# Kernel tuning notes

Hardware: AMD Instinct MI355X
Metric: run time of the kernel (lower is better)

## Reference

```python
import jax, jax.numpy as jnp
import numpy as np

H = 24
HEAD_DIM = 128
EPS = 1e-6
IP_SCALE = 1.0

def _rms(x, w):
    return x * jax.lax.rsqrt(jnp.mean(x * x, axis=-1, keepdims=True) + EPS) * w

def _heads(x, B):
    # (B, S, H*D) -> (B, H, S, D)
    return x.reshape(B, x.shape[1], H, HEAD_DIM).transpose(0, 2, 1, 3)

def _merge(x):
    B, h, S, d = x.shape
    return x.transpose(0, 2, 1, 3).reshape(B, S, h * d)

def _sdpa(q, k, v):
    s = jnp.einsum('bhqd,bhkd->bhqk', q, k) * (1.0 / np.sqrt(HEAD_DIM))
    return jnp.einsum('bhqk,bhkd->bhqd', jax.nn.softmax(s, axis=-1), v)

def _rope(x, cos, sin):
    # Flux-style real rotary: interleaved pairs, out = x*cos + rot(x)*sin
    xr = x.reshape(x.shape[:-1] + (-1, 2))
    x1, x2 = xr[..., 0], xr[..., 1]
    xrot = jnp.stack([-x2, x1], axis=-1).reshape(x.shape)
    return x * cos + xrot * sin

def setup_inputs():
    key = jax.random.key(0)
    ks = jax.random.split(key, 24)
    B, S_img, L_txt, D, IP_DIM, N_IP = 1, 2048, 512, 3072, 2048, 1024
    S = S_img + L_txt
    def w(k, i, o):
        return jax.random.normal(k, (i, o), jnp.float32) * 0.02
    def b(k, o):
        return jax.random.normal(k, (o,), jnp.float32) * 0.01
    pos = jnp.arange(S, dtype=jnp.float32)
    freqs = 1.0 / (10000.0 ** (jnp.arange(0, HEAD_DIM, 2, dtype=jnp.float32) / HEAD_DIM))
    ang = pos[:, None] * freqs[None, :]
    cos = jnp.repeat(jnp.cos(ang), 2, axis=-1)  # (S, HEAD_DIM)
    sin = jnp.repeat(jnp.sin(ang), 2, axis=-1)
    return {
        'hidden_states': jax.random.normal(ks[0], (B, S_img, D), jnp.float32),
        'encoder_hidden_states': jax.random.normal(ks[1], (B, L_txt, D), jnp.float32),
        'ip_hidden_states': jax.random.normal(ks[2], (B, N_IP, IP_DIM), jnp.float32),
        'rot_cos': cos, 'rot_sin': sin,
        'Wq': w(ks[3], D, D), 'bq': b(ks[4], D),
        'Wk': w(ks[5], D, D), 'bk': b(ks[6], D),
        'Wv': w(ks[7], D, D), 'bv': b(ks[8], D),
        'norm_q_w': jnp.ones((HEAD_DIM,), jnp.float32),
        'norm_k_w': jnp.ones((HEAD_DIM,), jnp.float32),
        'aWq': w(ks[9], D, D), 'abq': b(ks[10], D),
        'aWk': w(ks[11], D, D), 'abk': b(ks[12], D),
        'aWv': w(ks[13], D, D), 'abv': b(ks[14], D),
        'norm_aq_w': jnp.ones((HEAD_DIM,), jnp.float32),
        'norm_ak_w': jnp.ones((HEAD_DIM,), jnp.float32),
        'Wk_ip': w(ks[15], IP_DIM, D), 'bk_ip': b(ks[16], D),
        'Wv_ip': w(ks[17], IP_DIM, D), 'bv_ip': b(ks[18], D),
        'norm_ipq_w': jnp.ones((HEAD_DIM,), jnp.float32),
        'norm_ipk_w': jnp.ones((HEAD_DIM,), jnp.float32),
        'Wo': w(ks[19], D, D), 'bo': b(ks[20], D),
        'Wao': w(ks[21], D, D), 'bao': b(ks[22], D),
    }

def reference(hidden_states, encoder_hidden_states, ip_hidden_states, rot_cos, rot_sin,
              Wq, bq, Wk, bk, Wv, bv, norm_q_w, norm_k_w,
              aWq, abq, aWk, abk, aWv, abv, norm_aq_w, norm_ak_w,
              Wk_ip, bk_ip, Wv_ip, bv_ip, norm_ipq_w, norm_ipk_w,
              Wo, bo, Wao, bao):
    B, S_img, D = hidden_states.shape
    L = encoder_hidden_states.shape[1]
    q = _heads(hidden_states @ Wq + bq, B)   # (B,H,S_img,d)
    k = _heads(hidden_states @ Wk + bk, B)
    v = _heads(hidden_states @ Wv + bv, B)
    # IP-adapter cross-attention: RMS-normed raw image query vs projected image tokens
    ip_q = _rms(q, norm_ipq_w)
    ip_k = _rms(_heads(ip_hidden_states @ Wk_ip + bk_ip, B), norm_ipk_w)
    ip_v = _heads(ip_hidden_states @ Wv_ip + bv_ip, B)
    ip_out = _merge(_sdpa(ip_q, ip_k, ip_v))  # (B, S_img, D)
    # main joint attention with per-head QK RMSNorm
    q = _rms(q, norm_q_w)
    k = _rms(k, norm_k_w)
    eq = _rms(_heads(encoder_hidden_states @ aWq + abq, B), norm_aq_w)
    ek = _rms(_heads(encoder_hidden_states @ aWk + abk, B), norm_ak_w)
    ev = _heads(encoder_hidden_states @ aWv + abv, B)
    q = jnp.concatenate([eq, q], axis=2)
    k = jnp.concatenate([ek, k], axis=2)
    v = jnp.concatenate([ev, v], axis=2)
    q = _rope(q, rot_cos, rot_sin)
    k = _rope(k, rot_cos, rot_sin)
    hs = _merge(_sdpa(q, k, v))  # (B, L+S_img, D)
    enc = hs[:, :L]
    img = hs[:, L:] + IP_SCALE * ip_out
    img = img @ Wo + bo
    enc = enc @ Wao + bao
    return (img, enc)
```

## Files before the change

kernel.cpp:

```cpp
#include <hip/hip_runtime.h>
#include <hip/hip_bf16.h>
#include <cmath>
#include <cstdint>

#define H_    24
#define HD_   128
#define D_    3072
#define SIMG_ 2048
#define LTXT_ 512
#define SALL_ 2560
#define NIP_  1024
#define IPD_  2048

using bf16 = __hip_bfloat16;
typedef __bf16 bf16x8 __attribute__((ext_vector_type(8)));
typedef float  f32x4  __attribute__((ext_vector_type(4)));
typedef short  short8 __attribute__((ext_vector_type(8)));

#define QSCALE_ 0.12751741f

#define SWZ_BLOCK(bx, by)                                              \
  {                                                                    \
    int _gx = gridDim.x;                                               \
    int _hw = blockIdx.x + blockIdx.y * _gx;                           \
    int _n  = _gx * gridDim.y;                                         \
    int _lid = (_hw & 7) * (_n >> 3) + (_hw >> 3);                     \
    bx = _lid % _gx;                                                   \
    by = _lid / _gx;                                                   \
  }

__device__ __forceinline__ unsigned short f2bf(float f) {
  unsigned int u = __float_as_uint(f);
  unsigned int r = (u + 0x7fffu + ((u >> 16) & 1u)) >> 16;
  return (unsigned short)r;
}
__device__ __forceinline__ float bf2f(unsigned short u) {
  return __uint_as_float(((unsigned int)u) << 16);
}

__device__ __forceinline__ void gload16(const void* g, void* l) {
  __builtin_amdgcn_global_load_lds(
      (const __attribute__((address_space(1))) unsigned*)g,
      (__attribute__((address_space(3))) unsigned*)l, 16, 0, 0);
}

__global__ void cast_kernel(const float* __restrict__ x, unsigned short* __restrict__ y, int n4) {
  int i = blockIdx.x * blockDim.x + threadIdx.x;
  if (i >= n4) return;
  float4 v = reinterpret_cast<const float4*>(x)[i];
  ushort4 o = make_ushort4(f2bf(v.x), f2bf(v.y), f2bf(v.z), f2bf(v.w));
  reinterpret_cast<ushort4*>(y)[i] = o;
}

__global__ __launch_bounds__(512)
void transpose_cast3_kernel(const float* __restrict__ W0, const float* __restrict__ W1,
                            const float* __restrict__ W2, unsigned short* __restrict__ Wt,
                            int R, int C) {
  __shared__ float tile[32][69];
  const float* W = blockIdx.z == 0 ? W0 : (blockIdx.z == 1 ? W1 : W2);
  unsigned short* dst = Wt + (size_t)blockIdx.z * R * C;
  int bx = blockIdx.x * 64, by = blockIdx.y * 32;
  int tx = threadIdx.x, ty = threadIdx.y;
#pragma unroll
  for (int i = 0; i < 4; i++)
    tile[ty + 8 * i][tx] = W[(size_t)(by + ty + 8 * i) * C + bx + tx];
  __syncthreads();
  int t = ty * 64 + tx;
  int colr = t >> 3;
  int r0 = (t & 7) * 4;
  ushort4 o = make_ushort4(f2bf(tile[r0][colr]), f2bf(tile[r0 + 1][colr]),
                           f2bf(tile[r0 + 2][colr]), f2bf(tile[r0 + 3][colr]));
  *reinterpret_cast<ushort4*>(&dst[(size_t)(bx + colr) * R + by + r0]) = o;
}

__device__ __forceinline__ void gemm_core(const bf16* __restrict__ Ab, const bf16* __restrict__ Bb,
                                          int K, bf16* Alds, bf16* Blds, int t,
                                          int wid, int l16, int lg, f32x4 (&acc)[2][8]) {
  char* AldsB = (char*)Alds + t * 16;
  char* BldsB = (char*)Blds + t * 16;
  for (int kt = 0; kt < K; kt += 32) {
    __syncthreads();
    gload16(Ab + kt,                    AldsB);
    gload16(Ab + (size_t)64 * K + kt,   AldsB + 4096);
    gload16(Bb + kt,                    BldsB);
    gload16(Bb + (size_t)64 * K + kt,   BldsB + 4096);
    __syncthreads();
    bf16x8 af[2], bfr[8];
#pragma unroll
    for (int mi = 0; mi < 2; mi++)
      af[mi] = *reinterpret_cast<const bf16x8*>(&Alds[(wid * 32 + mi * 16 + l16) * 32 + lg * 8]);
#pragma unroll
    for (int ni = 0; ni < 8; ni++)
      bfr[ni] = *reinterpret_cast<const bf16x8*>(&Blds[(ni * 16 + l16) * 32 + lg * 8]);
    __builtin_amdgcn_s_setprio(1);
#pragma unroll
    for (int mi = 0; mi < 2; mi++)
#pragma unroll
      for (int ni = 0; ni < 8; ni++)
        acc[mi][ni] = __builtin_amdgcn_mfma_f32_16x16x32_bf16(af[mi], bfr[ni], acc[mi][ni], 0, 0, 0);
    __builtin_amdgcn_s_setprio(0);
  }
}

__global__ __launch_bounds__(256)
void gemm_proj_kernel(const bf16* __restrict__ A, const bf16* __restrict__ Wt,
                      int M, int K, int projmap,
                      const float* __restrict__ b0, const float* __restrict__ b1,
                      const float* __restrict__ b2,
                      const float* __restrict__ rcos, const float* __restrict__ rsin,
                      int pos_off, int tok_off, int Sout,
                      unsigned short* __restrict__ qa_p, const float* __restrict__ nq,
                      unsigned short* __restrict__ ipq_p, const float* __restrict__ nipq, int Sip,
                      unsigned short* __restrict__ ka_p, const float* __restrict__ nk,
                      unsigned short* __restrict__ va_p) {
  __shared__ __align__(16) bf16 Alds[128 * 32];
  __shared__ __align__(16) bf16 Blds[128 * 32];
  __shared__ __align__(16) bf16 VtS[64 * 128];
  int t = threadIdx.x;
  int lane = t & 63, wid = t >> 6;
  int l16 = lane & 15, lg = lane >> 4;
  int bx, by;
  SWZ_BLOCK(bx, by);
  int bm = bx * 128;
  int proj = by / 24, head = by % 24;
  int code = (projmap >> (proj * 4)) & 15;
  int arow = t >> 2, aseg = t & 3;

  f32x4 acc[2][8];
#pragma unroll
  for (int i = 0; i < 2; i++)
#pragma unroll
    for (int j = 0; j < 8; j++) { acc[i][j][0]=0.f; acc[i][j][1]=0.f; acc[i][j][2]=0.f; acc[i][j][3]=0.f; }

  const bf16* Ab = A  + (size_t)(bm + arow) * K + aseg * 8;
  const bf16* Bb = Wt + (size_t)(by * 128 + arow) * K + aseg * 8;
  gemm_core(Ab, Bb, K, Alds, Blds, t, wid, l16, lg, acc);

  const float* bias = proj == 0 ? b0 : (proj == 1 ? b1 : b2);
  int bcol = head * 128;

  if (code == 2) {
#pragma unroll
    for (int half = 0; half < 2; half++) {
      __syncthreads();
#pragma unroll
      for (int mi = 0; mi < 2; mi++)
#pragma unroll
        for (int j = 0; j < 4; j++) {
          int tok = wid * 32 + mi * 16 + lg * 4 + j;
#pragma unroll
          for (int ni = 0; ni < 4; ni++) {
            int col = l16 + 16 * ni;
            float val = acc[mi][ni + 4 * half][j] + bias[bcol + col + 64 * half];
            unsigned short uv = f2bf(val);
            VtS[col * 128 + (tok ^ ((col & 15) << 3))] = *(bf16*)&uv;
          }
        }
      __syncthreads();
      int colr = t >> 2;
      int tokbase = (t & 3) * 32;
#pragma unroll
      for (int it = 0; it < 4; it++) {
        int tok0 = tokbase + it * 8;
        short8 vv = *reinterpret_cast<const short8*>(&VtS[colr * 128 + (tok0 ^ ((colr & 15) << 3))]);
        *reinterpret_cast<short8*>(
            &va_p[((size_t)head * HD_ + 64 * half + colr) * Sout + tok_off + bm + tok0]) = vv;
      }
    }
    return;
  }

#pragma unroll
  for (int mi = 0; mi < 2; mi++) {
#pragma unroll
    for (int j = 0; j < 4; j++) {
      int rloc = wid * 32 + mi * 16 + lg * 4 + j;
      int row  = bm + rloc;
      float v[8];
#pragma unroll
      for (int ni = 0; ni < 8; ni++)
        v[ni] = acc[mi][ni][j] + bias[bcol + l16 + 16 * ni];

      float ss = 0.f;
#pragma unroll
      for (int ni = 0; ni < 8; ni++) ss += v[ni] * v[ni];
#pragma unroll
      for (int off = 1; off < 16; off <<= 1) ss += __shfl_xor(ss, off);
      float rr = rsqrtf(ss * (1.f / 128.f) + 1e-6f);

      auto emit = [&](unsigned short* outp, const float* nw, int rope, int scale,
                      int toff, int So) {
        float y[8];
#pragma unroll
        for (int ni = 0; ni < 8; ni++) {
          int col = l16 + 16 * ni;
          y[ni] = v[ni] * rr * nw[col];
        }
        if (rope) {
#pragma unroll
          for (int ni = 0; ni < 8; ni++) {
            int col = l16 + 16 * ni;
            float c  = rcos[(size_t)(pos_off + row) * HD_ + col];
            float sn = rsin[(size_t)(pos_off + row) * HD_ + col];
            float partner = __shfl_xor(y[ni], 1);
            y[ni] = y[ni] * c + ((col & 1) ? partner : -partner) * sn;
          }
        }
        if (scale) {
#pragma unroll
          for (int ni = 0; ni < 8; ni++) y[ni] *= QSCALE_;
        }
#pragma unroll
        for (int ni = 0; ni < 8; ni++) {
          int col = l16 + 16 * ni;
          outp[((size_t)head * So + toff + row) * HD_ + col] = f2bf(y[ni]);
        }
      };

      if (code == 0) {
        emit(qa_p, nq, 1, 1, tok_off, Sout);
        if (ipq_p) emit(ipq_p, nipq, 0, 1, 0, Sip);
      } else if (code == 1) {
        emit(ka_p, nk, 1, 0, tok_off, Sout);
      } else {
        emit(ka_p, nk, 0, 0, tok_off, Sout);
      }
    }
  }
}

__global__ __launch_bounds__(256)
void gemm_out2_kernel(const bf16* __restrict__ A_img, const bf16* __restrict__ A_enc,
                      const bf16* __restrict__ Wt,
                      const float* __restrict__ bo, const float* __restrict__ bao,
                      float* __restrict__ C_img, float* __restrict__ C_enc) {
  __shared__ __align__(16) bf16 Alds[128 * 32];
  __shared__ __align__(16) bf16 Blds[128 * 32];
  int t = threadIdx.x;
  int lane = t & 63, wid = t >> 6;
  int l16 = lane & 15, lg = lane >> 4;
  int bx, byn;
  SWZ_BLOCK(bx, byn);
  int is_enc = bx >= 16;
  const bf16* A = is_enc ? A_enc : A_img;
  const bf16* W = Wt + (is_enc ? (size_t)D_ * D_ : 0);
  const float* bias = is_enc ? bao : bo;
  float* C = is_enc ? C_enc : C_img;
  int bm = (is_enc ? bx - 16 : bx) * 128;
  int bn = byn * 128;
  int arow = t >> 2, aseg = t & 3;
  const int K = D_;

  f32x4 acc[2][8];
#pragma unroll
  for (int i = 0; i < 2; i++)
#pragma unroll
    for (int j = 0; j < 8; j++) { acc[i][j][0]=0.f; acc[i][j][1]=0.f; acc[i][j][2]=0.f; acc[i][j][3]=0.f; }

  const bf16* Ab = A + (size_t)(bm + arow) * K + aseg * 8;
  const bf16* Bb = W + (size_t)(bn + arow) * K + aseg * 8;
  gemm_core(Ab, Bb, K, Alds, Blds, t, wid, l16, lg, acc);

#pragma unroll
  for (int mi = 0; mi < 2; mi++)
#pragma unroll
    for (int j = 0; j < 4; j++) {
      int row = bm + wid * 32 + mi * 16 + lg * 4 + j;
#pragma unroll
      for (int ni = 0; ni < 8; ni++)
        C[(size_t)row * D_ + bn + l16 + 16 * ni] = acc[mi][ni][j] + bias[bn + l16 + 16 * ni];
    }
}

__global__ __launch_bounds__(256)
void attn_kernel(const bf16* __restrict__ Q1, const bf16* __restrict__ K1,
                 const bf16* __restrict__ Vt1, unsigned short* __restrict__ O1,
                 int Sq1, int Skv1, int nx1,
                 const bf16* __restrict__ Q2, const bf16* __restrict__ K2,
                 const bf16* __restrict__ Vt2, unsigned short* __restrict__ O2,
                 int Sq2, int Skv2) {
  __shared__ __align__(16) bf16 Kl[64 * 128];
  __shared__ __align__(16) bf16 Vl[128 * 64];
  int t = threadIdx.x, lane = t & 63, wid = t >> 6;
  int l16 = lane & 15, lg = lane >> 4;
  int bx, h;
  SWZ_BLOCK(bx, h);
  int is2 = bx >= nx1;
  const bf16* Q  = is2 ? Q2  : Q1;
  const bf16* K  = is2 ? K2  : K1;
  const bf16* Vt = is2 ? Vt2 : Vt1;
  unsigned short* O = is2 ? O2 : O1;
  int Sq  = is2 ? Sq2  : Sq1;
  int Skv = is2 ? Skv2 : Skv1;
  int qb = (is2 ? bx - nx1 : bx) * 128 + wid * 32;

  const bf16* Qh  = Q  + (size_t)h * Sq * HD_;
  const bf16* Kh  = K  + (size_t)h * Skv * HD_;
  const bf16* Vth = Vt + (size_t)h * HD_ * Skv;

  bf16x8 qf[2][4];
#pragma unroll
  for (int m = 0; m < 2; m++)
#pragma unroll
    for (int kb = 0; kb < 4; kb++)
      qf[m][kb] = *reinterpret_cast<const bf16x8*>(
          &Qh[(size_t)(qb + m * 16 + l16) * HD_ + lg * 8 + kb * 32]);

  f32x4 acc[2][8];
#pragma unroll
  for (int m = 0; m < 2; m++)
#pragma unroll
    for (int cb = 0; cb < 8; cb++) { acc[m][cb][0]=0.f; acc[m][cb][1]=0.f; acc[m][cb][2]=0.f; acc[m][cb][3]=0.f; }
  float l_r[2] = {0.f, 0.f};

  int ksrow = t >> 4, kscol = t & 15;
  int vsrow = t >> 3, vscol = t & 7;

  for (int kt = 0; kt < Skv; kt += 64) {
    __syncthreads();
#pragma unroll
    for (int p = 0; p < 4; p++) {
      int r = p * 16 + ksrow;
      short8 kv = *reinterpret_cast<const short8*>(&Kh[(size_t)(kt + r) * HD_ + kscol * 8]);
      *reinterpret_cast<short8*>((char*)Kl + r * 256 + ((kscol * 16) ^ ((r & 7) << 4))) = kv;
    }
#pragma unroll
    for (int p = 0; p < 4; p++) {
      int d = p * 32 + vsrow;
      short8 vv = *reinterpret_cast<const short8*>(&Vth[(size_t)d * Skv + kt + vscol * 8]);
      *reinterpret_cast<short8*>((char*)Vl + d * 128 + ((vscol * 16) ^ ((d & 7) << 4))) = vv;
    }
    __syncthreads();

    f32x4 sc[2][4];
#pragma unroll
    for (int m = 0; m < 2; m++)
#pragma unroll
      for (int nb = 0; nb < 4; nb++) { sc[m][nb][0]=0.f; sc[m][nb][1]=0.f; sc[m][nb][2]=0.f; sc[m][nb][3]=0.f; }
    __builtin_amdgcn_s_setprio(1);
#pragma unroll
    for (int kb = 0; kb < 4; kb++) {
#pragma unroll
      for (int nb = 0; nb < 4; nb++) {
        int r = nb * 16 + l16;
        bf16x8 kf = *reinterpret_cast<const bf16x8*>(
            (char*)Kl + r * 256 + ((lg * 16 + kb * 64) ^ ((r & 7) << 4)));
        sc[0][nb] = __builtin_amdgcn_mfma_f32_16x16x32_bf16(kf, qf[0][kb], sc[0][nb], 0, 0, 0);
        sc[1][nb] = __builtin_amdgcn_mfma_f32_16x16x32_bf16(kf, qf[1][kb], sc[1][nb], 0, 0, 0);
      }
    }
    __builtin_amdgcn_s_setprio(0);
    __syncthreads();

#pragma unroll
    for (int m = 0; m < 2; m++) {
      float part = 0.f;
#pragma unroll
      for (int nb = 0; nb < 4; nb++)
#pragma unroll
        for (int j = 0; j < 4; j++) {
          float p = exp2f(sc[m][nb][j]);
          sc[m][nb][j] = p;
          part += p;
        }
      l_r[m] += part;
      char* Pb = (char*)Kl + (wid * 2 + m) * 2048 + l16 * 128;
#pragma unroll
      for (int nb = 0; nb < 4; nb++) {
#pragma unroll
        for (int w = 0; w < 2; w++) {
          unsigned int pk;
          asm("v_cvt_pk_bf16_f32 %0, %1, %2"
              : "=v"(pk) : "v"(sc[m][nb][2 * w]), "v"(sc[m][nb][2 * w + 1]));
          int colb = nb * 32 + lg * 8 + w * 4;
          *(unsigned int*)(Pb + (colb ^ ((l16 & 7) << 4))) = pk;
        }
      }
    }
    asm volatile("s_waitcnt lgkmcnt(0)" ::: "memory");

#pragma unroll
    for (int kb2 = 0; kb2 < 2; kb2++) {
      bf16x8 pa[2];
#pragma unroll
      for (int m = 0; m < 2; m++)
        pa[m] = *reinterpret_cast<const bf16x8*>(
            (char*)Kl + (wid * 2 + m) * 2048 + l16 * 128 + ((lg * 16 + kb2 * 64) ^ ((l16 & 7) << 4)));
      __builtin_amdgcn_s_setprio(1);
#pragma unroll
      for (int cb = 0; cb < 8; cb++) {
        int d = cb * 16 + l16;
        bf16x8 vf = *reinterpret_cast<const bf16x8*>(
            (char*)Vl + d * 128 + ((lg * 16 + kb2 * 64) ^ ((d & 7) << 4)));
        acc[0][cb] = __builtin_amdgcn_mfma_f32_16x16x32_bf16(pa[0], vf, acc[0][cb], 0, 0, 0);
        acc[1][cb] = __builtin_amdgcn_mfma_f32_16x16x32_bf16(pa[1], vf, acc[1][cb], 0, 0, 0);
      }
      __builtin_amdgcn_s_setprio(0);
    }
  }

#pragma unroll
  for (int m = 0; m < 2; m++) {
    l_r[m] += __shfl_xor(l_r[m], 16);
    l_r[m] += __shfl_xor(l_r[m], 32);
  }

#pragma unroll
  for (int m = 0; m < 2; m++) {
    float inv[4];
#pragma unroll
    for (int j = 0; j < 4; j++) inv[j] = 1.0f / __shfl(l_r[m], lg * 4 + j);
#pragma unroll
    for (int cb = 0; cb < 8; cb++) {
      int col = h * HD_ + l16 + 16 * cb;
#pragma unroll
      for (int j = 0; j < 4; j++) {
        int row = qb + m * 16 + lg * 4 + j;
        O[(size_t)row * (H_ * HD_) + col] = f2bf(acc[m][cb][j] * inv[j]);
      }
    }
  }
}

__global__ void combine_kernel(const unsigned short* __restrict__ attn,
                               const unsigned short* __restrict__ ipo,
                               unsigned short* __restrict__ img_in) {
  size_t i = ((size_t)blockIdx.x * blockDim.x + threadIdx.x) * 8;
  if (i >= (size_t)SIMG_ * D_) return;
  short8 a = *reinterpret_cast<const short8*>(attn + (size_t)LTXT_ * D_ + i);
  short8 b = *reinterpret_cast<const short8*>(ipo + i);
  short8 o;
#pragma unroll
  for (int j = 0; j < 8; j++)
    o[j] = (short)f2bf(bf2f((unsigned short)a[j]) + bf2f((unsigned short)b[j]));
  *reinterpret_cast<short8*>(img_in + i) = o;
}

extern "C" void kernel_launch(void* const* d_in, const int* in_sizes, int n_in,
                              void* d_out, int out_size, void* d_ws, size_t ws_size,
                              hipStream_t stream) {
  const float* hs   = (const float*)d_in[0];
  const float* ehs  = (const float*)d_in[1];
  const float* iphs = (const float*)d_in[2];
  const float* rcos = (const float*)d_in[3];
  const float* rsin = (const float*)d_in[4];
  const float* Wq   = (const float*)d_in[5];  const float* bq   = (const float*)d_in[6];
  const float* Wk   = (const float*)d_in[7];  const float* bk   = (const float*)d_in[8];
  const float* Wv   = (const float*)d_in[9];  const float* bv   = (const float*)d_in[10];
  const float* nqw  = (const float*)d_in[11]; const float* nkw  = (const float*)d_in[12];
  const float* aWq  = (const float*)d_in[13]; const float* abq  = (const float*)d_in[14];
  const float* aWk  = (const float*)d_in[15]; const float* abk  = (const float*)d_in[16];
  const float* aWv  = (const float*)d_in[17]; const float* abv  = (const float*)d_in[18];
  const float* naqw = (const float*)d_in[19]; const float* nakw = (const float*)d_in[20];
  const float* Wkip = (const float*)d_in[21]; const float* bkip = (const float*)d_in[22];
  const float* Wvip = (const float*)d_in[23]; const float* bvip = (const float*)d_in[24];
  const float* nipqw= (const float*)d_in[25]; const float* nipkw= (const float*)d_in[26];
  const float* Wo   = (const float*)d_in[27]; const float* bo   = (const float*)d_in[28];
  const float* Wao  = (const float*)d_in[29]; const float* bao  = (const float*)d_in[30];
  float* out_img = (float*)d_out;
  float* out_enc = out_img + (size_t)SIMG_ * D_;

  char* ws = (char*)d_ws;
  bf16*  Wt      = (bf16*)(ws + 0);
  unsigned short* attn_bf   = (unsigned short*)(ws + 37748736);
  bf16*  qa      = (bf16*)(ws + 56623104);
  bf16*  ka      = (bf16*)(ws + 72351744);
  bf16*  vaT     = (bf16*)(ws + 88080384);
  bf16*  ipq_bf  = (bf16*)(ws + 103809024);
  bf16*  ipk_bf  = (bf16*)(ws + 116391936);
  bf16*  ipvT   = (bf16*)(ws + 122683392);
  bf16*  act_bf  = (bf16*)(ws + 128974848);
  unsigned short* ip_out_bf = (unsigned short*)act_bf;
  bf16*  img_in  = (bf16*)qa;
  if (ws_size < 141557760) return;

  dim3 tb(64, 8);

  cast_kernel<<<SIMG_ * D_ / 4 / 256, 256, 0, stream>>>(hs, (unsigned short*)act_bf, SIMG_ * D_ / 4);
  transpose_cast3_kernel<<<dim3(48, 96, 3), tb, 0, stream>>>(Wq, Wk, Wv, (unsigned short*)Wt, D_, D_);
  gemm_proj_kernel<<<dim3(16, 72), 256, 0, stream>>>(act_bf, Wt, SIMG_, D_, 0x210,
      bq, bk, bv, rcos, rsin, LTXT_, LTXT_, SALL_,
      (unsigned short*)qa, nqw, (unsigned short*)ipq_bf, nipqw, SIMG_,
      (unsigned short*)ka, nkw, (unsigned short*)vaT);

  cast_kernel<<<LTXT_ * D_ / 4 / 256, 256, 0, stream>>>(ehs, (unsigned short*)act_bf, LTXT_ * D_ / 4);
  transpose_cast3_kernel<<<dim3(48, 96, 3), tb, 0, stream>>>(aWq, aWk, aWv, (unsigned short*)Wt, D_, D_);
  gemm_proj_kernel<<<dim3(4, 72), 256, 0, stream>>>(act_bf, Wt, LTXT_, D_, 0x210,
      abq, abk, abv, rcos, rsin, 0, 0, SALL_,
      (unsigned short*)qa, naqw, nullptr, nipqw, SIMG_,
      (unsigned short*)ka, nakw, (unsigned short*)vaT);

  cast_kernel<<<NIP_ * IPD_ / 4 / 256, 256, 0, stream>>>(iphs, (unsigned short*)act_bf, NIP_ * IPD_ / 4);
  transpose_cast3_kernel<<<dim3(48, 64, 2), tb, 0, stream>>>(Wkip, Wvip, Wvip, (unsigned short*)Wt, IPD_, D_);
  gemm_proj_kernel<<<dim3(8, 48), 256, 0, stream>>>(act_bf, Wt, NIP_, IPD_, 0x23,
      bkip, bvip, bvip, nullptr, nullptr, 0, 0, NIP_,
      nullptr, nullptr, nullptr, nullptr, 0,
      (unsigned short*)ipk_bf, nipkw, (unsigned short*)ipvT);

  transpose_cast3_kernel<<<dim3(48, 96, 2), tb, 0, stream>>>(Wo, Wao, Wao, (unsigned short*)Wt, D_, D_);

  attn_kernel<<<dim3(SALL_ / 128 + SIMG_ / 128, H_), 256, 0, stream>>>(
      qa, ka, vaT, attn_bf, SALL_, SALL_, SALL_ / 128,
      ipq_bf, ipk_bf, ipvT, ip_out_bf, SIMG_, NIP_);

  combine_kernel<<<SIMG_ * D_ / 8 / 256, 256, 0, stream>>>(attn_bf, ip_out_bf, (unsigned short*)img_in);

  gemm_out2_kernel<<<dim3(20, 24), 256, 0, stream>>>(img_in, (const bf16*)attn_bf, Wt,
                                                     bo, bao, out_img, out_enc);
}
```

Measured before the change: 732.9 us.

## Double GEMM K-tile to 64 with XOR-swizzled LDS layout

The shared GEMM core now loads a 64-wide K slice per iteration instead of 32, halving the number of barrier pairs per K loop. The LDS layout for A and B uses an XOR swizzle on 16-byte chunks keyed by row, applied to both the global-load mapping and the fragment reads, to avoid bank conflicts with 128-byte rows. The projection kernel aliases its V-transpose scratch onto the enlarged A buffer to keep LDS usage bounded. The trade-off is more LDS per block and a single-buffered pipeline with larger load bursts.

Measured after the change: 670.7 us. 8.5% less time.

```diff
diff --git a/kernel.cpp b/kernel.cpp
--- a/kernel.cpp
+++ b/kernel.cpp
@@ -73,32 +73,42 @@
   *reinterpret_cast<ushort4*>(&dst[(size_t)(bx + colr) * R + by + r0]) = o;
 }
 
-__device__ __forceinline__ void gemm_core(const bf16* __restrict__ Ab, const bf16* __restrict__ Bb,
-                                          int K, bf16* Alds, bf16* Blds, int t,
-                                          int wid, int l16, int lg, f32x4 (&acc)[2][8]) {
+__device__ __forceinline__ void gemm_core64(const bf16* __restrict__ Ab, const bf16* __restrict__ Bb,
+                                            int K, bf16* Alds, bf16* Blds, int t,
+                                            int wid, int l16, int lg, f32x4 (&acc)[2][8]) {
   char* AldsB = (char*)Alds + t * 16;
   char* BldsB = (char*)Blds + t * 16;
-  for (int kt = 0; kt < K; kt += 32) {
+  for (int kt = 0; kt < K; kt += 64) {
     __syncthreads();
-    gload16(Ab + kt,                    AldsB);
-    gload16(Ab + (size_t)64 * K + kt,   AldsB + 4096);
-    gload16(Bb + kt,                    BldsB);
-    gload16(Bb + (size_t)64 * K + kt,   BldsB + 4096);
+#pragma unroll
+    for (int p = 0; p < 4; p++) {
+      gload16(Ab + (size_t)(32 * p) * K + kt, AldsB + p * 4096);
+      gload16(Bb + (size_t)(32 * p) * K + kt, BldsB + p * 4096);
+    }
     __syncthreads();
-    bf16x8 af[2], bfr[8];
-#pragma unroll
-    for (int mi = 0; mi < 2; mi++)
-      af[mi] = *reinterpret_cast<const bf16x8*>(&Alds[(wid * 32 + mi * 16 + l16) * 32 + lg * 8]);
-#pragma unroll
-    for (int ni = 0; ni < 8; ni++)
-      bfr[ni] = *reinterpret_cast<const bf16x8*>(&Blds[(ni * 16 + l16) * 32 + lg * 8]);
-    __builtin_amdgcn_s_setprio(1);
-#pragma unroll
-    for (int mi = 0; mi < 2; mi++)
-#pragma unroll
-      for (int ni = 0; ni < 8; ni++)
-        acc[mi][ni] = __builtin_amdgcn_mfma_f32_16x16x32_bf16(af[mi], bfr[ni], acc[mi][ni], 0, 0, 0);
-    __builtin_amdgcn_s_setprio(0);
+#pragma unroll
+    for (int kb = 0; kb < 2; kb++) {
+      bf16x8 af[2], bfr[8];
+#pragma unroll
+      for (int mi = 0; mi < 2; mi++) {
+        int r = wid * 32 + mi * 16 + l16;
+        af[mi] = *reinterpret_cast<const bf16x8*>(
+            (char*)Alds + r * 128 + ((lg * 16 + kb * 64) ^ ((r & 7) << 4)));
+      }
+#pragma unroll
+      for (int ni = 0; ni < 8; ni++) {
+        int r = ni * 16 + l16;
+        bfr[ni] = *reinterpret_cast<const bf16x8*>(
+            (char*)Blds + r * 128 + ((lg * 16 + kb * 64) ^ ((r & 7) << 4)));
+      }
+      __builtin_amdgcn_s_setprio(1);
+#pragma unroll
+      for (int mi = 0; mi < 2; mi++)
+#pragma unroll
+        for (int ni = 0; ni < 8; ni++)
+          acc[mi][ni] = __builtin_amdgcn_mfma_f32_16x16x32_bf16(af[mi], bfr[ni], acc[mi][ni], 0, 0, 0);
+      __builtin_amdgcn_s_setprio(0);
+    }
   }
 }
 
@@ -113,9 +123,9 @@
                       unsigned short* __restrict__ ipq_p, const float* __restrict__ nipq, int Sip,
                       unsigned short* __restrict__ ka_p, const float* __restrict__ nk,
                       unsigned short* __restrict__ va_p) {
-  __shared__ __align__(16) bf16 Alds[128 * 32];
-  __shared__ __align__(16) bf16 Blds[128 * 32];
-  __shared__ __align__(16) bf16 VtS[64 * 128];
+  __shared__ __align__(16) bf16 Alds[128 * 64];
+  __shared__ __align__(16) bf16 Blds[128 * 64];
+  bf16* VtS = Alds;
   int t = threadIdx.x;
   int lane = t & 63, wid = t >> 6;
   int l16 = lane & 15, lg = lane >> 4;
@@ -124,7 +134,8 @@
   int bm = bx * 128;
   int proj = by / 24, head = by % 24;
   int code = (projmap >> (proj * 4)) & 15;
-  int arow = t >> 2, aseg = t & 3;
+  int arow = t >> 3;
+  int aseg = (t & 7) ^ (arow & 7);
 
   f32x4 acc[2][8];
 #pragma unroll
@@ -134,7 +145,7 @@
 
   const bf16* Ab = A  + (size_t)(bm + arow) * K + aseg * 8;
   const bf16* Bb = Wt + (size_t)(by * 128 + arow) * K + aseg * 8;
-  gemm_core(Ab, Bb, K, Alds, Blds, t, wid, l16, lg, acc);
+  gemm_core64(Ab, Bb, K, Alds, Blds, t, wid, l16, lg, acc);
 
   const float* bias = proj == 0 ? b0 : (proj == 1 ? b1 : b2);
   int bcol = head * 128;
@@ -234,8 +245,8 @@
                       const bf16* __restrict__ Wt,
                       const float* __restrict__ bo, const float* __restrict__ bao,
                       float* __restrict__ C_img, float* __restrict__ C_enc) {
-  __shared__ __align__(16) bf16 Alds[128 * 32];
-  __shared__ __align__(16) bf16 Blds[128 * 32];
+  __shared__ __align__(16) bf16 Alds[128 * 64];
+  __shared__ __align__(16) bf16 Blds[128 * 64];
   int t = threadIdx.x;
   int lane = t & 63, wid = t >> 6;
   int l16 = lane & 15, lg = lane >> 4;
@@ -248,7 +259,8 @@
   float* C = is_enc ? C_enc : C_img;
   int bm = (is_enc ? bx - 16 : bx) * 128;
   int bn = byn * 128;
-  int arow = t >> 2, aseg = t & 3;
+  int arow = t >> 3;
+  int aseg = (t & 7) ^ (arow & 7);
   const int K = D_;
 
   f32x4 acc[2][8];
@@ -259,7 +271,7 @@
 
   const bf16* Ab = A + (size_t)(bm + arow) * K + aseg * 8;
   const bf16* Bb = W + (size_t)(bn + arow) * K + aseg * 8;
-  gemm_core(Ab, Bb, K, Alds, Blds, t, wid, l16, lg, acc);
+  gemm_core64(Ab, Bb, K, Alds, Blds, t, wid, l16, lg, acc);
 
 #pragma unroll
   for (int mi = 0; mi < 2; mi++)
```
